# Kernel tuning notes

Measured on AMD Instinct MI355X. Metric: run time of the kernel, lower is better.

Reference implementation:

```python
import jax, jax.numpy as jnp
import numpy as np

PRIME_DELAYS = (1, 2, 3, 5)
LOCAL_LR = 0.05  # base_local_lr after clamp to [0, 0.99]


def _apply_delays(x, delay_gains):
    """OCNS phasal delay embedding. x: [B,T,D,2], delay_gains: [n_delays,D,2]."""
    x_eff = x
    for idx, tau in enumerate(PRIME_DELAYS):
        gr = delay_gains[idx, :, 0]
        gi = delay_gains[idx, :, 1]
        dr = x[:, :-tau, :, 0]
        di = x[:, :-tau, :, 1]
        upd = jnp.stack([dr * gr - di * gi, dr * gi + di * gr], axis=-1)
        x_eff = x_eff.at[:, tau:].add(upd)
    return x_eff


def _moe_expert_choice(xf, gate_bias, W_router, W1, W2, capacity):
    """Expert-choice MoE: each expert picks its top-`capacity` tokens.
    xf: [N,F] flattened complex features; returns [N,F]."""
    logits = xf @ W_router + gate_bias              # [N,E]
    scores = jax.nn.softmax(logits, axis=-1)        # [N,E]
    topv, topi = jax.lax.top_k(scores.T, capacity)  # each [E,C]
    xe = xf[topi]                                   # [E,C,F] gather
    h = jax.nn.gelu(jnp.einsum('ecf,efh->ech', xe, W1))
    ye = jnp.einsum('ech,ehf->ecf', h, W2) * topv[..., None]
    N, F = xf.shape
    return jnp.zeros((N, F), xf.dtype).at[topi.reshape(-1)].add(ye.reshape(-1, F))


def _forward(x_stream, delay_gains, Wg_spec, W_router, W1, W2, cos_p, sin_p, local_iters):
    x = jnp.nan_to_num(x_stream.astype(jnp.float32))
    B, T, D, _ = x.shape
    N = B * T
    E = W_router.shape[1]
    capacity = (2 * N) // E  # top-2-equivalent expert-choice token budget

    # spectral gate bias: per-token spectral magnitude -> expert logit bias [N,E]
    mag = jnp.sqrt(x[..., 0] ** 2 + x[..., 1] ** 2 + 1e-8)
    gate_bias = mag.reshape(N, D) @ Wg_spec

    # phase-rotated target: x_target[:, t] = rot(x[:, t-1]); x_target[:, 0] = x[:, 0]
    prev = x[:, :-1]
    rot_r = prev[..., 0] * cos_p - prev[..., 1] * sin_p
    rot_i = prev[..., 0] * sin_p + prev[..., 1] * cos_p
    x_target = jnp.concatenate([x[:, :1], jnp.stack([rot_r, rot_i], axis=-1)], axis=1)

    def step(xc, _):
        x_eff = _apply_delays(xc, delay_gains)
        pred = _moe_expert_choice(x_eff.reshape(N, 2 * D), gate_bias, W_router, W1, W2, capacity)
        pred = pred.reshape(B, T, D, 2)
        upd = jnp.clip(LOCAL_LR * (x_target - pred), -10.0, 10.0)
        return xc + upd, None

    out, _ = jax.lax.scan(step, x, None, length=local_iters)
    return out


def setup_inputs() -> dict:
    key = jax.random.key(0)
    ks = jax.random.split(key, 8)
    B, T, D, E = 2, 2048, 256, 64
    F = 2 * D
    phase = jax.random.uniform(ks[0], (D,)) * 2.0 * np.pi
    return {
        'x_stream': jax.random.normal(ks[1], (B, T, D, 2), jnp.float32) * 0.5,
        'delay_gains': jax.random.normal(ks[2], (len(PRIME_DELAYS), D, 2), jnp.float32) * 0.02,
        'Wg_spec': jax.random.normal(ks[3], (D, E), jnp.float32) / np.sqrt(D),
        'W_router': jax.random.normal(ks[4], (F, E), jnp.float32) / np.sqrt(F),
        'W1': jax.random.normal(ks[5], (E, F, F), jnp.float32) / np.sqrt(F),
        'W2': jax.random.normal(ks[6], (E, F, F), jnp.float32) / np.sqrt(F),
        'cos_p': jnp.cos(phase),
        'sin_p': jnp.sin(phase),
        'local_iters': 8,
    }


def reference(x_stream, delay_gains, Wg_spec, W_router, W1, W2, cos_p, sin_p, local_iters):
    return _forward(x_stream, delay_gains, Wg_spec, W_router, W1, W2, cos_p, sin_p, local_iters)
```

## Files before the change

kernel.cpp:

```cpp
#include <hip/hip_runtime.h>
#include <hip/hip_bf16.h>

#define TB 2
#define TT 2048
#define TD 256
#define TE 64
#define TF 512
#define TN 4096
#define TCAP 128
#define NITER 8

typedef __attribute__((ext_vector_type(8))) short bf16x8;
typedef __attribute__((ext_vector_type(4))) float f32x4;

__device__ inline float sanitize(float v){
  if (v != v) return 0.0f;
  const float FMAX = 3.402823466e+38f;
  if (v >  FMAX) return  FMAX;
  if (v < -FMAX) return -FMAX;
  return v;
}

__device__ inline short f2bf(float f){
  union { __hip_bfloat16 h; short s; } u;
  u.h = __float2bfloat16(f);
  return u.s;
}

__device__ inline float gelu_tanh(float x){
  float x3 = x*x*x;
  return 0.5f*x*(1.0f + tanhf(0.7978845608028654f*(x + 0.044715f*x3)));
}

__device__ __forceinline__ void gload16(const void* g, void* l){
  __builtin_amdgcn_global_load_lds(
      (__attribute__((address_space(1))) void*)g,
      (__attribute__((address_space(3))) void*)l, 16, 0, 0);
}


__global__ void k_init(const float* __restrict__ xs, const float* __restrict__ cosp,
                       const float* __restrict__ sinp, float* __restrict__ xw,
                       float* __restrict__ xt){
  int idx = blockIdx.x*256 + threadIdx.x;
  if (idx >= TN*TD) return;
  int d = idx & (TD-1);
  int n = idx >> 8;
  int t = n & (TT-1);
  float xr = sanitize(xs[2*idx]), xi = sanitize(xs[2*idx+1]);
  xw[2*idx] = xr; xw[2*idx+1] = xi;
  float tr, ti;
  if (t == 0){ tr = xr; ti = xi; }
  else {
    float pr = sanitize(xs[2*(idx-TD)]), pi = sanitize(xs[2*(idx-TD)+1]);
    float c = cosp[d], s = sinp[d];
    tr = pr*c - pi*s;
    ti = pr*s + pi*c;
  }
  xt[2*idx] = tr; xt[2*idx+1] = ti;
}

__global__ __launch_bounds__(64) void k_gatebias(const float* __restrict__ xw,
                                                 const float* __restrict__ wg,
                                                 float* __restrict__ gb){
  __shared__ float mag[TD];
  int n = blockIdx.x, t = threadIdx.x;
  for (int d = t; d < TD; d += 64){
    float xr = xw[(size_t)n*TF + 2*d], xi = xw[(size_t)n*TF + 2*d + 1];
    mag[d] = sqrtf(xr*xr + xi*xi + 1e-8f);
  }
  __syncthreads();
  float acc = 0.f;
  for (int d = 0; d < TD; d++) acc += mag[d]*wg[d*TE + t];
  gb[(size_t)n*TE + t] = acc;
}

__global__ __launch_bounds__(256) void k_castw(const float* __restrict__ W, short* __restrict__ Wt){
  __shared__ float tile[64][68];
  int e = blockIdx.y;
  int kt = (blockIdx.x >> 3) * 64;
  int nt = (blockIdx.x & 7) * 64;
  int tid = threadIdx.x;
  {
    int row = tid >> 4;
    int c4 = (tid & 15) * 4;
    #pragma unroll
    for (int i = 0; i < 4; i++){
      int r = row + i*16;
      float4 v = *(const float4*)(W + ((size_t)e*TF + kt + r)*TF + nt + c4);
      *(float4*)&tile[r][c4] = v;
    }
  }
  __syncthreads();
  #pragma unroll
  for (int i = 0; i < 2; i++){
    int un = tid + i*256;
    int nrow = un >> 3;
    int k8 = (un & 7) * 8;
    bf16x8 o;
    #pragma unroll
    for (int j = 0; j < 8; j++) o[j] = f2bf(tile[k8+j][nrow]);
    *(bf16x8*)(Wt + ((size_t)e*TF + nt + nrow)*TF + kt + k8) = o;
  }
}


__device__ __forceinline__ void gather16(const float* __restrict__ ye,
                                         const int* __restrict__ cnt,
                                         const int* __restrict__ list,
                                         int nrow, int kq, float* p){
  #pragma unroll
  for (int q = 0; q < 16; q++) p[q] = 0.f;
  int c = cnt[nrow];
  for (int j = 0; j < c; j++){
    int row = list[nrow*64 + j];
    const float4* s = (const float4*)(ye + (size_t)row*TF + kq);
    #pragma unroll
    for (int k4 = 0; k4 < 4; k4++){
      float4 v = s[k4];
      p[4*k4+0] += v.x; p[4*k4+1] += v.y; p[4*k4+2] += v.z; p[4*k4+3] += v.w;
    }
  }
}

__device__ __forceinline__ void load_row16(const float* __restrict__ xw,
                                           const float* __restrict__ xt,
                                           const float* __restrict__ ye,
                                           const int* __restrict__ cnt,
                                           const int* __restrict__ list,
                                           int nrow, int kq, int upd, float* o){
  size_t off = (size_t)nrow*TF + kq;
  const float4* a4 = (const float4*)(xw + off);
  if (upd){
    float p[16];
    gather16(ye, cnt, list, nrow, kq, p);
    const float4* t4 = (const float4*)(xt + off);
    #pragma unroll
    for (int j = 0; j < 4; j++){
      float4 a = a4[j], t = t4[j];
      float u;
      u = 0.05f*(t.x - p[4*j+0]); u = fminf(10.f, fmaxf(-10.f, u)); o[4*j+0] = a.x + u;
      u = 0.05f*(t.y - p[4*j+1]); u = fminf(10.f, fmaxf(-10.f, u)); o[4*j+1] = a.y + u;
      u = 0.05f*(t.z - p[4*j+2]); u = fminf(10.f, fmaxf(-10.f, u)); o[4*j+2] = a.z + u;
      u = 0.05f*(t.w - p[4*j+3]); u = fminf(10.f, fmaxf(-10.f, u)); o[4*j+3] = a.w + u;
    }
  } else {
    #pragma unroll
    for (int j = 0; j < 4; j++){
      float4 a = a4[j];
      o[4*j+0] = a.x; o[4*j+1] = a.y; o[4*j+2] = a.z; o[4*j+3] = a.w;
    }
  }
}

__global__ __launch_bounds__(256) void k_fuse(
    const float* __restrict__ xOld, float* __restrict__ xNew,
    const float* __restrict__ xt, const float* __restrict__ ye,
    const int* __restrict__ cnt, const int* __restrict__ list,
    const float* __restrict__ g, const float* __restrict__ wr,
    const float* __restrict__ gb, short* __restrict__ xbf,
    float* __restrict__ scoresT, int upd)
{
  __shared__ float xeff[8][516];
  __shared__ float Bt[64][68];
  int tid = threadIdx.x;
  int tok = tid >> 5;
  int kq  = (tid & 31) * 16;
  int n   = blockIdx.x*8 + tok;
  int t   = n & (TT-1);
  size_t rowoff = (size_t)n*TF + kq;

  float cur[16], eff[16];
  load_row16(xOld, xt, ye, cnt, list, n, kq, upd, cur);
  #pragma unroll
  for (int q = 0; q < 16; q++) eff[q] = cur[q];
  const int taus[4] = {1,2,3,5};
  int d0 = kq >> 1;
  #pragma unroll
  for (int i = 0; i < 4; i++){
    int tau = taus[i];
    if (t >= tau){
      float nb[16];
      load_row16(xOld, xt, ye, cnt, list, n - tau, kq, upd, nb);
      #pragma unroll
      for (int p = 0; p < 8; p++){
        float gr = g[2*(i*TD + d0 + p)];
        float gi = g[2*(i*TD + d0 + p) + 1];
        eff[2*p]   += nb[2*p]*gr - nb[2*p+1]*gi;
        eff[2*p+1] += nb[2*p]*gi + nb[2*p+1]*gr;
      }
    }
  }
  {
    float4* xn = (float4*)(xNew + rowoff);
    #pragma unroll
    for (int j = 0; j < 4; j++)
      xn[j] = make_float4(cur[4*j], cur[4*j+1], cur[4*j+2], cur[4*j+3]);
    bf16x8 o0, o1;
    #pragma unroll
    for (int q = 0; q < 8; q++){ o0[q] = f2bf(eff[q]); o1[q] = f2bf(eff[8+q]); }
    *(bf16x8*)(xbf + rowoff)     = o0;
    *(bf16x8*)(xbf + rowoff + 8) = o1;
    #pragma unroll
    for (int j = 0; j < 4; j++)
      *(float4*)&xeff[tok][kq + 4*j] = make_float4(eff[4*j], eff[4*j+1], eff[4*j+2], eff[4*j+3]);
  }
  __syncthreads();

  int tx = tid & 31;
  float acc0 = gb[(size_t)n*TE + 2*tx];
  float acc1 = gb[(size_t)n*TE + 2*tx + 1];
  int rB = tid >> 2, c16 = (tid & 3)*16;
  for (int kk = 0; kk < TF; kk += 64){
    #pragma unroll
    for (int jj = 0; jj < 4; jj++)
      *(float4*)&Bt[rB][c16 + 4*jj] = *(const float4*)(wr + (size_t)(kk+rB)*TE + c16 + 4*jj);
    __syncthreads();
    #pragma unroll
    for (int k = 0; k < 64; k++){
      float a = xeff[tok][kk + k];
      float2 b = *(const float2*)&Bt[k][2*tx];
      acc0 += a*b.x; acc1 += a*b.y;
    }
    __syncthreads();
  }
  float m = fmaxf(acc0, acc1);
  #pragma unroll
  for (int off = 1; off < 32; off <<= 1) m = fmaxf(m, __shfl_xor(m, off));
  float e0 = expf(acc0 - m), e1 = expf(acc1 - m);
  float s = e0 + e1;
  #pragma unroll
  for (int off = 1; off < 32; off <<= 1) s += __shfl_xor(s, off);
  float inv = 1.0f / s;
  scoresT[(size_t)(2*tx)*TN + n]     = e0*inv;
  scoresT[(size_t)(2*tx+1)*TN + n]   = e1*inv;
}

__global__ __launch_bounds__(1024) void k_topk2(const float* __restrict__ scoresT,
                                                int* __restrict__ topi, float* __restrict__ topv,
                                                int* __restrict__ cnt){
  int e = blockIdx.x;
  const float* sc = scoresT + (size_t)e*TN;
  __shared__ unsigned int hist[4096];
  __shared__ unsigned int chunkSum[64];
  __shared__ unsigned int s_prefix;
  __shared__ int s_k, s_cnt, s_min;
  int tid = threadIdx.x;
  if (tid < 64) cnt[e*64 + tid] = 0;
  unsigned int u[4];
  #pragma unroll
  for (int i = 0; i < 4; i++) u[i] = __float_as_uint(sc[tid + i*1024]);
  if (tid == 0){ s_prefix = 0u; s_k = TCAP; }

  const int shifts[3]  = {20, 8, 0};
  const int nbins[3]   = {4096, 4096, 256};
  const unsigned int pmasks[3] = {0u, 0xFFF00000u, 0xFFFFFF00u};
  for (int r = 0; r < 3; r++){
    int shift = shifts[r], nb = nbins[r];
    unsigned int bmask = (unsigned)nb - 1u;
    int logC = (nb == 4096) ? 6 : 2;
    for (int i = tid; i < nb; i += 1024) hist[i] = 0u;
    if (tid < 64) chunkSum[tid] = 0u;
    __syncthreads();
    unsigned int pref = s_prefix;
    unsigned int pmask = pmasks[r];
    #pragma unroll
    for (int i = 0; i < 4; i++)
      if ((u[i] & pmask) == pref) atomicAdd(&hist[(u[i] >> shift) & bmask], 1u);
    __syncthreads();
    for (int b = tid; b < nb; b += 1024){
      unsigned int h = hist[b];
      if (h) atomicAdd(&chunkSum[b >> logC], h);
    }
    __syncthreads();
    if (tid < 64){
      int chunk = 63 - tid;
      unsigned int s = chunkSum[chunk];
      unsigned int scan = s;
      #pragma unroll
      for (int d = 1; d < 64; d <<= 1){
        unsigned int t = __shfl_up(scan, d);
        if (tid >= d) scan += t;
      }
      unsigned int excl = scan - s;
      int k = s_k;
      if (excl < (unsigned)k && scan >= (unsigned)k){
        int C = 1 << logC;
        unsigned int cum = excl;
        for (int b = C-1; b >= 0; b--){
          unsigned int h = hist[(chunk << logC) + b];
          cum += h;
          if (cum >= (unsigned)k){
            s_k = k - (int)(cum - h);
            s_prefix = pref | ((unsigned)((chunk << logC) + b) << shift);
            break;
          }
        }
      }
    }
    __syncthreads();
  }
  unsigned int thr = s_prefix;
  int need_eq = s_k;
  if (tid == 0) s_cnt = 0;
  __syncthreads();
  #pragma unroll
  for (int i = 0; i < 4; i++){
    if (u[i] > thr){
      int p = atomicAdd(&s_cnt, 1);
      topi[e*TCAP + p] = tid + i*1024;
      topv[e*TCAP + p] = __uint_as_float(u[i]);
    }
  }
  __syncthreads();
  int base = s_cnt;
  int last = -1;
  for (int i = 0; i < need_eq; i++){
    __syncthreads();
    if (tid == 0) s_min = TN;
    __syncthreads();
    #pragma unroll
    for (int j = 0; j < 4; j++){
      int n = tid + j*1024;
      if (u[j] == thr && n > last) atomicMin(&s_min, n);
    }
    __syncthreads();
    int nsel = s_min;
    if (tid == 0){ topi[e*TCAP + base + i] = nsel; topv[e*TCAP + base + i] = __uint_as_float(thr); }
    last = nsel;
  }
}


__global__ __launch_bounds__(256) void k_gemm1c(const short* __restrict__ xbf,
                                                const short* __restrict__ W1t,
                                                const int* __restrict__ topi,
                                                short* __restrict__ hbf,
                                                int* __restrict__ cnt,
                                                int* __restrict__ list){
  __shared__ __align__(16) short As[3][128*32];
  __shared__ __align__(16) short Bs[3][64*32];
  __shared__ int rows[128];
  int bid = blockIdx.x;
  int swz = (bid & 7)*64 + (bid >> 3);
  int e = swz >> 3, n0 = (swz & 7)*64;
  int tid = threadIdx.x;
  if (tid < 128) rows[tid] = topi[e*TCAP + tid];
  __syncthreads();
  if (n0 == 0 && tid < 128){
    int n = rows[tid];
    int slot = atomicAdd(&cnt[n], 1);
    list[n*64 + slot] = e*TCAP + tid;
  }
  int r4 = tid >> 2;
  int cs = (((tid & 3) ^ ((r4 >> 1) & 3)))*8;
  const short* sA0 = xbf + (size_t)rows[r4]*TF + cs;
  const short* sA1 = xbf + (size_t)rows[r4 + 64]*TF + cs;
  const short* sB  = W1t + ((size_t)e*TF + n0 + r4)*TF + cs;

  int w = tid >> 6, l = tid & 63;
  int lr = l & 15, lh = l >> 4;
  int ch = (lh ^ ((lr >> 1) & 3))*8;
  int aOff0 = (32*w + lr)*32 + ch;
  int aOff1 = aOff0 + 16*32;
  int bOff0 = lr*32 + ch;

  f32x4 acc[2][4];
  #pragma unroll
  for (int m = 0; m < 2; m++)
    #pragma unroll
    for (int j = 0; j < 4; j++)
      #pragma unroll
      for (int r = 0; r < 4; r++) acc[m][j][r] = 0.f;

  gload16(sA0, &As[0][tid*8]);
  gload16(sA1, &As[0][2048 + tid*8]);
  gload16(sB,  &Bs[0][tid*8]);
  gload16(sA0 + 32, &As[1][tid*8]);
  gload16(sA1 + 32, &As[1][2048 + tid*8]);
  gload16(sB  + 32, &Bs[1][tid*8]);

  int cur = 0;
  for (int t16 = 0; t16 < 16; t16++){
    if (t16 < 14){
      int kk = (t16+2)*32;
      int ld = cur + 2; if (ld >= 3) ld -= 3;
      gload16(sA0 + kk, &As[ld][tid*8]);
      gload16(sA1 + kk, &As[ld][2048 + tid*8]);
      gload16(sB  + kk, &Bs[ld][tid*8]);
      asm volatile("s_waitcnt vmcnt(6)" ::: "memory");
    } else if (t16 == 14){
      asm volatile("s_waitcnt vmcnt(3)" ::: "memory");
    } else {
      asm volatile("s_waitcnt vmcnt(0)" ::: "memory");
    }
    __builtin_amdgcn_sched_barrier(0);
    __builtin_amdgcn_s_barrier();
    __builtin_amdgcn_sched_barrier(0);
    bf16x8 a0 = *(const bf16x8*)&As[cur][aOff0];
    bf16x8 a1 = *(const bf16x8*)&As[cur][aOff1];
    #pragma unroll
    for (int j = 0; j < 4; j++){
      bf16x8 b = *(const bf16x8*)&Bs[cur][bOff0 + j*16*32];
      acc[0][j] = __builtin_amdgcn_mfma_f32_16x16x32_bf16(a0, b, acc[0][j], 0, 0, 0);
      acc[1][j] = __builtin_amdgcn_mfma_f32_16x16x32_bf16(a1, b, acc[1][j], 0, 0, 0);
    }
    __builtin_amdgcn_sched_barrier(0);
    __builtin_amdgcn_s_barrier();
    cur++; if (cur >= 3) cur = 0;
  }
  short* hdst = hbf + (size_t)e*TCAP*TF;
  #pragma unroll
  for (int m = 0; m < 2; m++)
    #pragma unroll
    for (int j = 0; j < 4; j++)
      #pragma unroll
      for (int r = 0; r < 4; r++){
        int row = 32*w + 16*m + lh*4 + r;
        int col = n0 + 16*j + lr;
        hdst[(size_t)row*TF + col] = f2bf(gelu_tanh(acc[m][j][r]));
      }
}

__global__ __launch_bounds__(256) void k_gemm2c(const short* __restrict__ hbf,
                                                const short* __restrict__ W2t,
                                                const int* __restrict__ topi,
                                                const float* __restrict__ topv,
                                                float* __restrict__ ye){
  __shared__ __align__(16) short As[3][128*32];
  __shared__ __align__(16) short Bs[3][64*32];
  __shared__ float tv[128];
  int bid = blockIdx.x;
  int swz = (bid & 7)*64 + (bid >> 3);
  int e = swz >> 3, n0 = (swz & 7)*64;
  int tid = threadIdx.x;
  if (tid < 128) tv[tid] = topv[e*TCAP + tid];
  __syncthreads();
  int r4 = tid >> 2;
  int cs = (((tid & 3) ^ ((r4 >> 1) & 3)))*8;
  const short* sA0 = hbf + ((size_t)e*TCAP + r4)*TF + cs;
  const short* sA1 = sA0 + (size_t)64*TF;
  const short* sB  = W2t + ((size_t)e*TF + n0 + r4)*TF + cs;

  int w = tid >> 6, l = tid & 63;
  int lr = l & 15, lh = l >> 4;
  int ch = (lh ^ ((lr >> 1) & 3))*8;
  int aOff0 = (32*w + lr)*32 + ch;
  int aOff1 = aOff0 + 16*32;
  int bOff0 = lr*32 + ch;

  f32x4 acc[2][4];
  #pragma unroll
  for (int m = 0; m < 2; m++)
    #pragma unroll
    for (int j = 0; j < 4; j++)
      #pragma unroll
      for (int r = 0; r < 4; r++) acc[m][j][r] = 0.f;

  gload16(sA0, &As[0][tid*8]);
  gload16(sA1, &As[0][2048 + tid*8]);
  gload16(sB,  &Bs[0][tid*8]);
  gload16(sA0 + 32, &As[1][tid*8]);
  gload16(sA1 + 32, &As[1][2048 + tid*8]);
  gload16(sB  + 32, &Bs[1][tid*8]);

  int cur = 0;
  for (int t16 = 0; t16 < 16; t16++){
    if (t16 < 14){
      int kk = (t16+2)*32;
      int ld = cur + 2; if (ld >= 3) ld -= 3;
      gload16(sA0 + kk, &As[ld][tid*8]);
      gload16(sA1 + kk, &As[ld][2048 + tid*8]);
      gload16(sB  + kk, &Bs[ld][tid*8]);
      asm volatile("s_waitcnt vmcnt(6)" ::: "memory");
    } else if (t16 == 14){
      asm volatile("s_waitcnt vmcnt(3)" ::: "memory");
    } else {
      asm volatile("s_waitcnt vmcnt(0)" ::: "memory");
    }
    __builtin_amdgcn_sched_barrier(0);
    __builtin_amdgcn_s_barrier();
    __builtin_amdgcn_sched_barrier(0);
    bf16x8 a0 = *(const bf16x8*)&As[cur][aOff0];
    bf16x8 a1 = *(const bf16x8*)&As[cur][aOff1];
    #pragma unroll
    for (int j = 0; j < 4; j++){
      bf16x8 b = *(const bf16x8*)&Bs[cur][bOff0 + j*16*32];
      acc[0][j] = __builtin_amdgcn_mfma_f32_16x16x32_bf16(a0, b, acc[0][j], 0, 0, 0);
      acc[1][j] = __builtin_amdgcn_mfma_f32_16x16x32_bf16(a1, b, acc[1][j], 0, 0, 0);
    }
    __builtin_amdgcn_sched_barrier(0);
    __builtin_amdgcn_s_barrier();
    cur++; if (cur >= 3) cur = 0;
  }
  float* ydst = ye + (size_t)e*TCAP*TF;
  #pragma unroll
  for (int m = 0; m < 2; m++)
    #pragma unroll
    for (int j = 0; j < 4; j++)
      #pragma unroll
      for (int r = 0; r < 4; r++){
        int row = 32*w + 16*m + lh*4 + r;
        int col = n0 + 16*j + lr;
        ydst[(size_t)row*TF + col] = acc[m][j][r] * tv[row];
      }
}

__global__ void k_final(float* __restrict__ out, const float* __restrict__ x,
                        const float* __restrict__ xt, const float* __restrict__ ye,
                        const int* __restrict__ cnt, const int* __restrict__ list){
  int i = blockIdx.x*256 + threadIdx.x;
  if (i >= TN*TF) return;
  int n = i >> 9;
  int f = i & (TF-1);
  float p = 0.f;
  int c = cnt[n];
  for (int j = 0; j < c; j++)
    p += ye[(size_t)list[n*64 + j]*TF + f];
  float u = 0.05f*(xt[i] - p);
  u = fminf(10.0f, fmaxf(-10.0f, u));
  out[i] = x[i] + u;
}

extern "C" void kernel_launch(void* const* d_in, const int* in_sizes, int n_in,
                              void* d_out, int out_size, void* d_ws, size_t ws_size,
                              hipStream_t stream){
  (void)in_sizes; (void)n_in; (void)out_size; (void)ws_size;
  const float* x_stream = (const float*)d_in[0];
  const float* gains    = (const float*)d_in[1];
  const float* Wg       = (const float*)d_in[2];
  const float* Wr       = (const float*)d_in[3];
  const float* W1       = (const float*)d_in[4];
  const float* W2       = (const float*)d_in[5];
  const float* cosp     = (const float*)d_in[6];
  const float* sinp     = (const float*)d_in[7];

  size_t off = 0;
  char* base = (char*)d_ws;
  auto alloc = [&](size_t bytes) -> void* {
    void* p = base + off;
    off += (bytes + 255) & ~(size_t)255;
    return p;
  };
  float* X0      = (float*)alloc((size_t)TN*TF*4);
  float* X1      = (float*)alloc((size_t)TN*TF*4);
  float* x_targ  = (float*)alloc((size_t)TN*TF*4);
  short* xf_bf   = (short*)alloc((size_t)TN*TF*2);
  float* gateb   = (float*)alloc((size_t)TN*TE*4);
  float* scoresT = (float*)alloc((size_t)TE*TN*4);
  int*   topi    = (int*)  alloc((size_t)TE*TCAP*4);
  float* topv    = (float*)alloc((size_t)TE*TCAP*4);
  short* h_bf    = (short*)alloc((size_t)TE*TCAP*TF*2);
  float* ye      = (float*)alloc((size_t)TE*TCAP*TF*4);
  int*   cnt     = (int*)  alloc((size_t)TN*4);
  int*   list    = (int*)  alloc((size_t)TN*64*4);
  short* W1t     = (short*)alloc((size_t)TE*TF*TF*2);
  short* W2t     = (short*)alloc((size_t)TE*TF*TF*2);

  k_init<<<(TN*TD + 255)/256, 256, 0, stream>>>(x_stream, cosp, sinp, X0, x_targ);
  k_gatebias<<<TN, 64, 0, stream>>>(X0, Wg, gateb);
  k_castw<<<dim3(64, TE), 256, 0, stream>>>(W1, W1t);
  k_castw<<<dim3(64, TE), 256, 0, stream>>>(W2, W2t);

  for (int it = 0; it < NITER; it++){
    const float* xO = (it & 1) ? X1 : X0;
    float*       xN = (it & 1) ? X0 : X1;
    k_fuse<<<TN/8, 256, 0, stream>>>(xO, xN, x_targ, ye, cnt, list, gains, Wr, gateb,
                                     xf_bf, scoresT, it > 0 ? 1 : 0);
    k_topk2<<<TE, 1024, 0, stream>>>(scoresT, topi, topv, cnt);
    k_gemm1c<<<TF/64*TE, 256, 0, stream>>>(xf_bf, W1t, topi, h_bf, cnt, list);
    k_gemm2c<<<TF/64*TE, 256, 0, stream>>>(h_bf, W2t, topi, topv, ye);
  }
  k_final<<<(TN*TF + 255)/256, 256, 0, stream>>>((float*)d_out, X0, x_targ, ye, cnt, list);
}
```

Before: 714.1 us.

## Split combine step out of fused delay kernel to avoid redundant scatter recomputation

The previous fused kernel recomputed the MoE combine (gather of expert outputs plus clipped update) for the current row and for each of four delayed neighbour rows, which is roughly five times the gather work. A separate k_combine kernel now materialises the updated state once, and k_fuse2 reads that state for the delay embedding and router. The final combine reuses the same kernel in place of k_final, and the shared-memory store order is rotated per lane to reduce bank conflicts. In exchange there is one extra launch per iteration and an extra write and read of the full state.

```diff
diff --git a/kernel.cpp b/kernel.cpp
--- a/kernel.cpp
+++ b/kernel.cpp
@@ -105,83 +105,81 @@
 }
 
 
-__device__ __forceinline__ void gather16(const float* __restrict__ ye,
-                                         const int* __restrict__ cnt,
-                                         const int* __restrict__ list,
-                                         int nrow, int kq, float* p){
+__global__ __launch_bounds__(256) void k_combine(
+    const float* __restrict__ xOld, float* __restrict__ xNew,
+    const float* __restrict__ xt, const float* __restrict__ ye,
+    const int* __restrict__ cnt, const int* __restrict__ list)
+{
+  int tid = threadIdx.x;
+  int tok = tid >> 5;
+  int kq  = (tid & 31) * 16;
+  int n   = blockIdx.x*8 + tok;
+  size_t off = (size_t)n*TF + kq;
+  float p[16];
   #pragma unroll
   for (int q = 0; q < 16; q++) p[q] = 0.f;
-  int c = cnt[nrow];
+  int c = cnt[n];
   for (int j = 0; j < c; j++){
-    int row = list[nrow*64 + j];
-    const float4* s = (const float4*)(ye + (size_t)row*TF + kq);
+    const float4* s = (const float4*)(ye + (size_t)list[n*64 + j]*TF + kq);
     #pragma unroll
     for (int k4 = 0; k4 < 4; k4++){
       float4 v = s[k4];
       p[4*k4+0] += v.x; p[4*k4+1] += v.y; p[4*k4+2] += v.z; p[4*k4+3] += v.w;
     }
   }
-}
-
-__device__ __forceinline__ void load_row16(const float* __restrict__ xw,
-                                           const float* __restrict__ xt,
-                                           const float* __restrict__ ye,
-                                           const int* __restrict__ cnt,
-                                           const int* __restrict__ list,
-                                           int nrow, int kq, int upd, float* o){
-  size_t off = (size_t)nrow*TF + kq;
-  const float4* a4 = (const float4*)(xw + off);
-  if (upd){
-    float p[16];
-    gather16(ye, cnt, list, nrow, kq, p);
-    const float4* t4 = (const float4*)(xt + off);
-    #pragma unroll
-    for (int j = 0; j < 4; j++){
-      float4 a = a4[j], t = t4[j];
-      float u;
-      u = 0.05f*(t.x - p[4*j+0]); u = fminf(10.f, fmaxf(-10.f, u)); o[4*j+0] = a.x + u;
-      u = 0.05f*(t.y - p[4*j+1]); u = fminf(10.f, fmaxf(-10.f, u)); o[4*j+1] = a.y + u;
-      u = 0.05f*(t.z - p[4*j+2]); u = fminf(10.f, fmaxf(-10.f, u)); o[4*j+2] = a.z + u;
-      u = 0.05f*(t.w - p[4*j+3]); u = fminf(10.f, fmaxf(-10.f, u)); o[4*j+3] = a.w + u;
-    }
-  } else {
-    #pragma unroll
-    for (int j = 0; j < 4; j++){
-      float4 a = a4[j];
-      o[4*j+0] = a.x; o[4*j+1] = a.y; o[4*j+2] = a.z; o[4*j+3] = a.w;
-    }
-  }
-}
-
-__global__ __launch_bounds__(256) void k_fuse(
-    const float* __restrict__ xOld, float* __restrict__ xNew,
-    const float* __restrict__ xt, const float* __restrict__ ye,
-    const int* __restrict__ cnt, const int* __restrict__ list,
-    const float* __restrict__ g, const float* __restrict__ wr,
-    const float* __restrict__ gb, short* __restrict__ xbf,
-    float* __restrict__ scoresT, int upd)
+  const float4* a4 = (const float4*)(xOld + off);
+  const float4* t4 = (const float4*)(xt + off);
+  float4* o4 = (float4*)(xNew + off);
+  #pragma unroll
+  for (int j = 0; j < 4; j++){
+    float4 a = a4[j], t = t4[j], o;
+    float u;
+    u = 0.05f*(t.x - p[4*j+0]); u = fminf(10.f, fmaxf(-10.f, u)); o.x = a.x + u;
+    u = 0.05f*(t.y - p[4*j+1]); u = fminf(10.f, fmaxf(-10.f, u)); o.y = a.y + u;
+    u = 0.05f*(t.z - p[4*j+2]); u = fminf(10.f, fmaxf(-10.f, u)); o.z = a.z + u;
+    u = 0.05f*(t.w - p[4*j+3]); u = fminf(10.f, fmaxf(-10.f, u)); o.w = a.w + u;
+    o4[j] = o;
+  }
+}
+
+
+__global__ __launch_bounds__(256) void k_fuse2(
+    const float* __restrict__ xcur, const float* __restrict__ g,
+    const float* __restrict__ wr, const float* __restrict__ gb,
+    short* __restrict__ xbf, float* __restrict__ scoresT)
 {
   __shared__ float xeff[8][516];
   __shared__ float Bt[64][68];
   int tid = threadIdx.x;
   int tok = tid >> 5;
-  int kq  = (tid & 31) * 16;
+  int lane5 = tid & 31;
+  int kq  = lane5 * 16;
   int n   = blockIdx.x*8 + tok;
   int t   = n & (TT-1);
   size_t rowoff = (size_t)n*TF + kq;
 
-  float cur[16], eff[16];
-  load_row16(xOld, xt, ye, cnt, list, n, kq, upd, cur);
-  #pragma unroll
-  for (int q = 0; q < 16; q++) eff[q] = cur[q];
+  float eff[16];
+  {
+    const float4* a4 = (const float4*)(xcur + rowoff);
+    #pragma unroll
+    for (int j = 0; j < 4; j++){
+      float4 v = a4[j];
+      eff[4*j+0] = v.x; eff[4*j+1] = v.y; eff[4*j+2] = v.z; eff[4*j+3] = v.w;
+    }
+  }
   const int taus[4] = {1,2,3,5};
   int d0 = kq >> 1;
   #pragma unroll
   for (int i = 0; i < 4; i++){
     int tau = taus[i];
     if (t >= tau){
+      const float4* b4 = (const float4*)(xcur + rowoff - (size_t)tau*TF);
       float nb[16];
-      load_row16(xOld, xt, ye, cnt, list, n - tau, kq, upd, nb);
+      #pragma unroll
+      for (int j = 0; j < 4; j++){
+        float4 v = b4[j];
+        nb[4*j+0] = v.x; nb[4*j+1] = v.y; nb[4*j+2] = v.z; nb[4*j+3] = v.w;
+      }
       #pragma unroll
       for (int p = 0; p < 8; p++){
         float gr = g[2*(i*TD + d0 + p)];
@@ -192,22 +190,21 @@
     }
   }
   {
-    float4* xn = (float4*)(xNew + rowoff);
-    #pragma unroll
-    for (int j = 0; j < 4; j++)
-      xn[j] = make_float4(cur[4*j], cur[4*j+1], cur[4*j+2], cur[4*j+3]);
     bf16x8 o0, o1;
     #pragma unroll
     for (int q = 0; q < 8; q++){ o0[q] = f2bf(eff[q]); o1[q] = f2bf(eff[8+q]); }
     *(bf16x8*)(xbf + rowoff)     = o0;
     *(bf16x8*)(xbf + rowoff + 8) = o1;
     #pragma unroll
-    for (int j = 0; j < 4; j++)
-      *(float4*)&xeff[tok][kq + 4*j] = make_float4(eff[4*j], eff[4*j+1], eff[4*j+2], eff[4*j+3]);
-  }
-  __syncthreads();
-
-  int tx = tid & 31;
+    for (int jj = 0; jj < 4; jj++){
+      int j = (jj + lane5) & 3;
+      *(float4*)&xeff[tok][kq + 4*j] =
+        make_float4(eff[4*j], eff[4*j+1], eff[4*j+2], eff[4*j+3]);
+    }
+  }
+  __syncthreads();
+
+  int tx = lane5;
   float acc0 = gb[(size_t)n*TE + 2*tx];
   float acc1 = gb[(size_t)n*TE + 2*tx + 1];
   int rB = tid >> 2, c16 = (tid & 3)*16;
@@ -504,22 +501,6 @@
         int col = n0 + 16*j + lr;
         ydst[(size_t)row*TF + col] = acc[m][j][r] * tv[row];
       }
-}
-
-__global__ void k_final(float* __restrict__ out, const float* __restrict__ x,
-                        const float* __restrict__ xt, const float* __restrict__ ye,
-                        const int* __restrict__ cnt, const int* __restrict__ list){
-  int i = blockIdx.x*256 + threadIdx.x;
-  if (i >= TN*TF) return;
-  int n = i >> 9;
-  int f = i & (TF-1);
-  float p = 0.f;
-  int c = cnt[n];
-  for (int j = 0; j < c; j++)
-    p += ye[(size_t)list[n*64 + j]*TF + f];
-  float u = 0.05f*(xt[i] - p);
-  u = fminf(10.0f, fmaxf(-10.0f, u));
-  out[i] = x[i] + u;
 }
 
 extern "C" void kernel_launch(void* const* d_in, const int* in_sizes, int n_in,
@@ -562,14 +543,17 @@
   k_castw<<<dim3(64, TE), 256, 0, stream>>>(W1, W1t);
   k_castw<<<dim3(64, TE), 256, 0, stream>>>(W2, W2t);
 
+  float* cur = X0;
+  float* nxt = X1;
   for (int it = 0; it < NITER; it++){
-    const float* xO = (it & 1) ? X1 : X0;
-    float*       xN = (it & 1) ? X0 : X1;
-    k_fuse<<<TN/8, 256, 0, stream>>>(xO, xN, x_targ, ye, cnt, list, gains, Wr, gateb,
-                                     xf_bf, scoresT, it > 0 ? 1 : 0);
+    if (it > 0){
+      k_combine<<<TN/8, 256, 0, stream>>>(cur, nxt, x_targ, ye, cnt, list);
+      float* tmp = cur; cur = nxt; nxt = tmp;
+    }
+    k_fuse2<<<TN/8, 256, 0, stream>>>(cur, gains, Wr, gateb, xf_bf, scoresT);
     k_topk2<<<TE, 1024, 0, stream>>>(scoresT, topi, topv, cnt);
     k_gemm1c<<<TF/64*TE, 256, 0, stream>>>(xf_bf, W1t, topi, h_bf, cnt, list);
     k_gemm2c<<<TF/64*TE, 256, 0, stream>>>(h_bf, W2t, topi, topv, ye);
   }
-  k_final<<<(TN*TF + 255)/256, 256, 0, stream>>>((float*)d_out, X0, x_targ, ye, cnt, list);
-}
+  k_combine<<<TN/8, 256, 0, stream>>>(cur, (float*)d_out, x_targ, ye, cnt, list);
+}
```

New measurement: 662.4 us. 1.08x faster.
